# Kernel optimization log

Hardware: AMD Instinct MI355X
Metric: run time of the kernel (lower is better)

The kernel has to match this reference:

```python
import jax, jax.numpy as jnp
import numpy as np

N, M, E, C_IN, C_OUT = 100000, 20000, 1600000, 128, 128


def _safe_inv(d):
    # 1/d with 0 where d==0 (matches PyG D[D==inf]=0), grad-safe
    safe = jnp.where(d > 0, d, 1.0)
    return jnp.where(d > 0, 1.0 / safe, 0.0)


def _hconv(x, node_idx, edge_idx, hw, W, b):
    # PyG HypergraphConv, use_attention=False, heads=1:
    # X' = D^{-1} H B^{-1} H^T (X Theta) + bias, D uses hyperedge_weight
    xt = x @ W  # [N, C_OUT]
    D = jax.ops.segment_sum(hw[edge_idx], node_idx, num_segments=N)
    Dinv = _safe_inv(D)  # [N]
    Bc = jax.ops.segment_sum(jnp.ones((E,), dtype=x.dtype), edge_idx, num_segments=M)
    Binv = _safe_inv(Bc)  # [M]
    # node -> hyperedge (message weighted by B^{-1} of target edge)
    e = jax.ops.segment_sum(Binv[edge_idx][:, None] * xt[node_idx], edge_idx, num_segments=M)
    # hyperedge -> node (message weighted by D^{-1} of target node)
    out = jax.ops.segment_sum(Dinv[node_idx][:, None] * e[edge_idx], node_idx, num_segments=N)
    return out + b


def setup_inputs() -> dict:
    key = jax.random.key(0)
    ks = jax.random.split(key, 12)
    x = jax.random.normal(ks[0], (N, C_IN), dtype=jnp.float32)
    node_idx = jax.random.randint(ks[1], (E,), 0, N, dtype=jnp.int32)
    edge_idx = jax.random.randint(ks[2], (E,), 0, M, dtype=jnp.int32)
    hyperedge_index = jnp.stack([node_idx, edge_idx])
    hyperedge_weight = jax.random.uniform(ks[3], (M,), dtype=jnp.float32) + 0.5
    hyperedge_attr = jax.random.normal(ks[4], (M, C_IN), dtype=jnp.float32)
    batch = jnp.zeros((N,), dtype=jnp.int32)
    s1 = 1.0 / np.sqrt(C_IN)
    s2 = 1.0 / np.sqrt(C_OUT)
    W1 = jax.random.uniform(ks[5], (C_IN, C_OUT), minval=-s1, maxval=s1, dtype=jnp.float32)
    W2 = jax.random.uniform(ks[6], (C_OUT, C_OUT), minval=-s2, maxval=s2, dtype=jnp.float32)
    W3 = jax.random.uniform(ks[7], (C_OUT, C_OUT), minval=-s2, maxval=s2, dtype=jnp.float32)
    b1 = jax.random.uniform(ks[8], (C_OUT,), minval=-s1, maxval=s1, dtype=jnp.float32)
    b2 = jax.random.uniform(ks[9], (C_OUT,), minval=-s2, maxval=s2, dtype=jnp.float32)
    b3 = jax.random.uniform(ks[10], (C_OUT,), minval=-s2, maxval=s2, dtype=jnp.float32)
    return {"x": x, "hyperedge_index": hyperedge_index, "hyperedge_weight": hyperedge_weight,
            "hyperedge_attr": hyperedge_attr, "batch": batch,
            "W1": W1, "b1": b1, "W2": W2, "b2": b2, "W3": W3, "b3": b3}


def reference(x, hyperedge_index, hyperedge_weight, hyperedge_attr, batch,
              W1, b1, W2, b2, W3, b3):
    node_idx = hyperedge_index[0]
    edge_idx = hyperedge_index[1]
    # dropout is identity in eval mode; hyperedge_attr/batch unused (no attention)
    h = jax.nn.relu(_hconv(x, node_idx, edge_idx, hyperedge_weight, W1, b1))
    h = jax.nn.relu(_hconv(h, node_idx, edge_idx, hyperedge_weight, W2, b2))
    h = jax.nn.relu(_hconv(h, node_idx, edge_idx, hyperedge_weight, W3, b3))
    return h
```

## Files before the change

kernel.cpp:

```cpp
#include <hip/hip_runtime.h>
#include <hip/hip_fp16.h>

#define NN 100000
#define MM 20000
#define EE 1600000

#define NBLK_E 256
#define CHUNK_E (EE / NBLK_E)
#define NBLK_N 128
#define CHUNK_N (EE / NBLK_N)
#define NRANGE2 50000

#define SCAN_BLOCK 256
#define SCAN_ITEMS 8
#define SCAN_TILE (SCAN_BLOCK * SCAN_ITEMS)
#define NB_E ((MM + SCAN_TILE - 1) / SCAN_TILE)
#define NB_N ((NN + SCAN_TILE - 1) / SCAN_TILE)
#define NB_TOT (NB_E + NB_N)

static inline size_t align256(size_t x) { return (x + 255) & ~(size_t)255; }

struct alignas(8) half4 { __half2 lo, hi; };

__device__ __forceinline__ float4 h4_to_f4(half4 v) {
  float2 a = __half22float2(v.lo);
  float2 b = __half22float2(v.hi);
  return make_float4(a.x, a.y, b.x, b.y);
}
__device__ __forceinline__ half4 f4_to_h4(float4 v) {
  half4 r;
  r.lo = __float22half2_rn(make_float2(v.x, v.y));
  r.hi = __float22half2_rn(make_float2(v.z, v.w));
  return r;
}

__global__ __launch_bounds__(256) void cvt_f2h_kernel(
    const float* __restrict__ in, __half* __restrict__ out, int n4) {
  int i = blockIdx.x * 256 + threadIdx.x;
  int stride = gridDim.x * 256;
  for (; i < n4; i += stride) {
    float4 v = ((const float4*)in)[i];
    ((half4*)out)[i] = f4_to_h4(v);
  }
}

__global__ __launch_bounds__(256) void ehist_kernel(
    const int* __restrict__ edge_idx,
    unsigned short* __restrict__ bcnt_e, unsigned short* __restrict__ lrank_e) {
  extern __shared__ int hist[];
  int b = blockIdx.x;
  for (int k = threadIdx.x; k < MM; k += 256) hist[k] = 0;
  __syncthreads();
  int lo = b * CHUNK_E, hi = lo + CHUNK_E;
  for (int i = lo + threadIdx.x; i < hi; i += 256) {
    int e = edge_idx[i];
    int r = atomicAdd(&hist[e], 1);
    lrank_e[i] = (unsigned short)r;
  }
  __syncthreads();
  unsigned short* row = bcnt_e + (size_t)b * MM;
  for (int k = threadIdx.x; k < MM / 2; k += 256) {
    ushort2 w;
    w.x = (unsigned short)hist[2 * k];
    w.y = (unsigned short)hist[2 * k + 1];
    ((ushort2*)row)[k] = w;
  }
}

__global__ __launch_bounds__(256) void nhist_kernel(
    const int* __restrict__ node_idx,
    unsigned short* __restrict__ bcnt_n, unsigned short* __restrict__ lrank_n) {
  extern __shared__ unsigned int histp[];
  int b = blockIdx.x;
  int lo = b * CHUNK_N, hi = lo + CHUNK_N;
  unsigned short* row = bcnt_n + (size_t)b * NN;
  for (int p = 0; p < 2; ++p) {
    int base = p * NRANGE2;
    for (int k = threadIdx.x; k < NRANGE2 / 2; k += 256) histp[k] = 0;
    __syncthreads();
    for (int i = lo + threadIdx.x; i < hi; i += 256) {
      int n = node_idx[i] - base;
      if ((unsigned)n < (unsigned)NRANGE2) {
        unsigned add = (n & 1) ? 0x10000u : 1u;
        unsigned old = atomicAdd(&histp[n >> 1], add);
        lrank_n[i] = (unsigned short)((old >> ((n & 1) * 16)) & 0xFFFFu);
      }
    }
    __syncthreads();
    for (int k = threadIdx.x; k < NRANGE2 / 2; k += 256) {
      unsigned w = histp[k];
      ushort2 o;
      o.x = (unsigned short)(w & 0xFFFFu);
      o.y = (unsigned short)(w >> 16);
      ((ushort2*)(row + base))[k] = o;
    }
    __syncthreads();
  }
}

__global__ __launch_bounds__(256) void colscan_kernel(
    unsigned short* __restrict__ bcnt_e, unsigned short* __restrict__ bcnt_n,
    int* __restrict__ ecnt, int* __restrict__ ncnt) {
  int i = blockIdx.x * 256 + threadIdx.x;
  if (i < MM) {
    int run = 0;
#pragma unroll 8
    for (int b = 0; b < NBLK_E; ++b) {
      size_t idx = (size_t)b * MM + i;
      int v = bcnt_e[idx];
      bcnt_e[idx] = (unsigned short)run;
      run += v;
    }
    ecnt[i] = run;
  } else if (i < MM + NN) {
    int n = i - MM;
    int run = 0;
#pragma unroll 8
    for (int b = 0; b < NBLK_N; ++b) {
      size_t idx = (size_t)b * NN + n;
      int v = bcnt_n[idx];
      bcnt_n[idx] = (unsigned short)run;
      run += v;
    }
    ncnt[n] = run;
  }
}

__global__ __launch_bounds__(SCAN_BLOCK) void scan_partial_kernel(
    const int* __restrict__ ecnt, const int* __restrict__ ncnt,
    int* __restrict__ eptr, int* __restrict__ nptr, int* __restrict__ bsum) {
  __shared__ int lds[SCAN_BLOCK];
  int b = blockIdx.x;
  const int* cnt; int* ptr; int len; int lb;
  if (b < NB_E) { cnt = ecnt; ptr = eptr; len = MM; lb = b; }
  else          { cnt = ncnt; ptr = nptr; len = NN; lb = b - NB_E; }
  int t = threadIdx.x;
  int lo = lb * SCAN_TILE + t * SCAN_ITEMS;
  int v[SCAN_ITEMS];
  int s = 0;
#pragma unroll
  for (int j = 0; j < SCAN_ITEMS; ++j) {
    int idx = lo + j;
    v[j] = (idx < len) ? cnt[idx] : 0;
    s += v[j];
  }
  lds[t] = s;
  __syncthreads();
  for (int d = 1; d < SCAN_BLOCK; d <<= 1) {
    int o = (t >= d) ? lds[t - d] : 0;
    __syncthreads();
    lds[t] += o;
    __syncthreads();
  }
  int run = lds[t] - s;
#pragma unroll
  for (int j = 0; j < SCAN_ITEMS; ++j) {
    int idx = lo + j;
    if (idx < len) ptr[idx] = run;
    run += v[j];
  }
  if (t == SCAN_BLOCK - 1) bsum[b] = lds[t];
}

__global__ void scan_bsum_kernel(int* __restrict__ bsum) {
  int t = threadIdx.x;
  if (t == 0) {
    int run = 0;
    for (int i = 0; i < NB_E; ++i) { int c = bsum[i]; bsum[i] = run; run += c; }
  } else if (t == 1) {
    int run = 0;
    for (int i = NB_E; i < NB_TOT; ++i) { int c = bsum[i]; bsum[i] = run; run += c; }
  }
}

__global__ __launch_bounds__(SCAN_BLOCK) void scan_fixup_kernel(
    int* __restrict__ eptr, int* __restrict__ nptr,
    const int* __restrict__ ecnt, const int* __restrict__ bsum,
    float* __restrict__ Binv) {
  int b = blockIdx.x;
  int* ptr; int len; int lb; bool isE;
  if (b < NB_E) { ptr = eptr; len = MM; lb = b; isE = true; }
  else          { ptr = nptr; len = NN; lb = b - NB_E; isE = false; }
  int boff = bsum[b];
  int t = threadIdx.x;
  int lo = lb * SCAN_TILE + t * SCAN_ITEMS;
#pragma unroll
  for (int j = 0; j < SCAN_ITEMS; ++j) {
    int idx = lo + j;
    if (idx < len) {
      ptr[idx] += boff;
      if (isE) {
        int c = ecnt[idx];
        Binv[idx] = (c > 0) ? 1.0f / (float)c : 0.0f;
      }
    }
  }
  if (b == 0 && t == 0) { eptr[MM] = EE; nptr[NN] = EE; }
}

__global__ __launch_bounds__(256) void fill2_kernel(
    const int* __restrict__ node_idx, const int* __restrict__ edge_idx,
    const int* __restrict__ eptr, const int* __restrict__ nptr,
    const unsigned short* __restrict__ bcnt_e,
    const unsigned short* __restrict__ bcnt_n,
    const unsigned short* __restrict__ lrank_e,
    const unsigned short* __restrict__ lrank_n,
    int* __restrict__ edge_nodes, int* __restrict__ node_edges) {
  int i = blockIdx.x * 256 + threadIdx.x;
  if (i >= EE) return;
  int e = edge_idx[i];
  int n = node_idx[i];
  int be = i / CHUNK_E;
  int bn = i / CHUNK_N;
  int slotE = eptr[e] + (int)bcnt_e[(size_t)be * MM + e] + (int)lrank_e[i];
  edge_nodes[slotE] = n;
  int slotN = nptr[n] + (int)bcnt_n[(size_t)bn * NN + n] + (int)lrank_n[i];
  node_edges[slotN] = e;
}

__global__ __launch_bounds__(256) void dinv_csr_kernel(
    const int* __restrict__ nptr, const int* __restrict__ node_edges,
    const float* __restrict__ hw, float* __restrict__ Dinv) {
  int n = blockIdx.x * 256 + threadIdx.x;
  if (n >= NN) return;
  int lo = nptr[n], hi = nptr[n + 1];
  float d = 0.0f;
  for (int j = lo; j < hi; ++j) d += hw[node_edges[j]];
  Dinv[n] = (d > 0.0f) ? 1.0f / d : 0.0f;
}

__device__ __forceinline__ void fma4(float4& acc, float s, const float4& m) {
  acc.x += s * m.x;
  acc.y += s * m.y;
  acc.z += s * m.z;
  acc.w += s * m.w;
}

__global__ __launch_bounds__(256) void gemm128_kernel(
    const __half* __restrict__ X, const float* __restrict__ W,
    __half* __restrict__ Y, int nrows) {
  __shared__ float Wl[128 * 128];
  float4* Wl4 = (float4*)Wl;
  const float4* W4 = (const float4*)W;
  for (int i = threadIdx.x; i < 128 * 32; i += 256) Wl4[i] = W4[i];
  __syncthreads();

  int tc = threadIdx.x & 15;
  int tr = threadIdx.x >> 4;
  int base = blockIdx.x * 64;
  int r[4];
  bool v[4];
#pragma unroll
  for (int j = 0; j < 4; ++j) {
    int rr = base + tr + j * 16;
    v[j] = rr < nrows;
    r[j] = v[j] ? rr : 0;
  }
  float4 acc[4][2];
#pragma unroll
  for (int j = 0; j < 4; ++j) {
    acc[j][0] = make_float4(0.f, 0.f, 0.f, 0.f);
    acc[j][1] = make_float4(0.f, 0.f, 0.f, 0.f);
  }
#pragma unroll 4
  for (int k4 = 0; k4 < 32; ++k4) {
    float4 xv[4];
#pragma unroll
    for (int j = 0; j < 4; ++j)
      xv[j] = h4_to_f4(((const half4*)X)[(size_t)r[j] * 32 + k4]);
#pragma unroll
    for (int kk = 0; kk < 4; ++kk) {
      float4 wva = Wl4[(k4 * 4 + kk) * 32 + tc];
      float4 wvb = Wl4[(k4 * 4 + kk) * 32 + 16 + tc];
#pragma unroll
      for (int j = 0; j < 4; ++j) {
        float xk = ((const float*)&xv[j])[kk];
        fma4(acc[j][0], xk, wva);
        fma4(acc[j][1], xk, wvb);
      }
    }
  }
#pragma unroll
  for (int j = 0; j < 4; ++j) {
    if (v[j]) {
      ((half4*)Y)[(size_t)r[j] * 32 + tc] = f4_to_h4(acc[j][0]);
      ((half4*)Y)[(size_t)r[j] * 32 + 16 + tc] = f4_to_h4(acc[j][1]);
    }
  }
}

__global__ __launch_bounds__(256) void edge_agg_kernel(
    const __half* __restrict__ hin, const int* __restrict__ eptr,
    const int* __restrict__ edge_nodes, const float* __restrict__ Binv,
    __half* __restrict__ eout) {
  int half_id = threadIdx.x >> 5;
  int lane = threadIdx.x & 31;
  int m = blockIdx.x * 8 + half_id;
  if (m >= MM) return;
  int lo = eptr[m], hi = eptr[m + 1];
  const half4* h4p = (const half4*)hin;
  float4 acc = make_float4(0.f, 0.f, 0.f, 0.f);
  int j = lo;
  for (; j + 8 <= hi; j += 8) {
    int idx[8];
#pragma unroll
    for (int u = 0; u < 8; ++u) idx[u] = edge_nodes[j + u];
    float4 s[8];
#pragma unroll
    for (int u = 0; u < 8; ++u) s[u] = h4_to_f4(h4p[(size_t)idx[u] * 32 + lane]);
    acc.x += ((s[0].x + s[1].x) + (s[2].x + s[3].x)) + ((s[4].x + s[5].x) + (s[6].x + s[7].x));
    acc.y += ((s[0].y + s[1].y) + (s[2].y + s[3].y)) + ((s[4].y + s[5].y) + (s[6].y + s[7].y));
    acc.z += ((s[0].z + s[1].z) + (s[2].z + s[3].z)) + ((s[4].z + s[5].z) + (s[6].z + s[7].z));
    acc.w += ((s[0].w + s[1].w) + (s[2].w + s[3].w)) + ((s[4].w + s[5].w) + (s[6].w + s[7].w));
  }
  for (; j < hi; ++j) {
    int n = edge_nodes[j];
    float4 a = h4_to_f4(h4p[(size_t)n * 32 + lane]);
    acc.x += a.x; acc.y += a.y; acc.z += a.z; acc.w += a.w;
  }
  float bi = Binv[m];
  acc.x *= bi; acc.y *= bi; acc.z *= bi; acc.w *= bi;
  ((half4*)eout)[(size_t)m * 32 + lane] = f4_to_h4(acc);
}

__device__ __forceinline__ void strow_q(float* Y, size_t row, int q, float4 v) {
  ((float4*)Y)[row * 32 + q] = v;
}
__device__ __forceinline__ void strow_q(__half* Y, size_t row, int q, float4 v) {
  ((half4*)Y)[row * 32 + q] = f4_to_h4(v);
}

template <typename TOUT>
__global__ __launch_bounds__(256) void node_agg_half_kernel(
    const __half* __restrict__ ein, const int* __restrict__ nptr,
    const int* __restrict__ node_edges, const float* __restrict__ Dinv,
    const float* __restrict__ bias, TOUT* __restrict__ out, int c4) {
  int g = threadIdx.x >> 4;
  int gl = threadIdx.x & 15;
  int n = blockIdx.x * 16 + g;
  int q = c4 + gl;
  int lo = nptr[n], hi = nptr[n + 1];
  const half4* e4 = (const half4*)ein;
  float4 acc = make_float4(0.f, 0.f, 0.f, 0.f);
  int j = lo;
  for (; j + 4 <= hi; j += 4) {
    int m0 = node_edges[j + 0];
    int m1 = node_edges[j + 1];
    int m2 = node_edges[j + 2];
    int m3 = node_edges[j + 3];
    float4 a = h4_to_f4(e4[(size_t)m0 * 32 + q]);
    float4 b = h4_to_f4(e4[(size_t)m1 * 32 + q]);
    float4 c = h4_to_f4(e4[(size_t)m2 * 32 + q]);
    float4 d = h4_to_f4(e4[(size_t)m3 * 32 + q]);
    acc.x += (a.x + b.x) + (c.x + d.x);
    acc.y += (a.y + b.y) + (c.y + d.y);
    acc.z += (a.z + b.z) + (c.z + d.z);
    acc.w += (a.w + b.w) + (c.w + d.w);
  }
  for (; j < hi; ++j) {
    int m = node_edges[j];
    float4 a = h4_to_f4(e4[(size_t)m * 32 + q]);
    acc.x += a.x; acc.y += a.y; acc.z += a.z; acc.w += a.w;
  }
  float di = Dinv[n];
  float4 bb = ((const float4*)bias)[q];
  float4 rv;
  rv.x = fmaxf(di * acc.x + bb.x, 0.f);
  rv.y = fmaxf(di * acc.y + bb.y, 0.f);
  rv.z = fmaxf(di * acc.z + bb.z, 0.f);
  rv.w = fmaxf(di * acc.w + bb.w, 0.f);
  strow_q(out, (size_t)n, q, rv);
}

extern "C" void kernel_launch(void* const* d_in, const int* in_sizes, int n_in,
                              void* d_out, int out_size, void* d_ws, size_t ws_size,
                              hipStream_t stream) {
  const float* x = (const float*)d_in[0];
  const int* hidx = (const int*)d_in[1];
  const int* node_idx = hidx;
  const int* edge_idx = hidx + EE;
  const float* hw = (const float*)d_in[2];
  const float* W1 = (const float*)d_in[5];
  const float* b1 = (const float*)d_in[6];
  const float* W2 = (const float*)d_in[7];
  const float* b2 = (const float*)d_in[8];
  const float* W3 = (const float*)d_in[9];
  const float* b3 = (const float*)d_in[10];
  float* out = (float*)d_out;

  char* ws = (char*)d_ws;
  size_t off = 0;
  auto alloc = [&](size_t bytes) -> char* {
    char* p = ws + off;
    off = align256(off + bytes);
    return p;
  };
  __half* xh   = (__half*)alloc(sizeof(__half) * (size_t)NN * 128);
  __half* h    = (__half*)alloc(sizeof(__half) * (size_t)NN * 128);
  __half* eraw = (__half*)alloc(sizeof(__half) * (size_t)MM * 128);
  __half* et   = (__half*)alloc(sizeof(__half) * (size_t)MM * 128);
  unsigned short* bcnt_e = (unsigned short*)alloc(sizeof(short) * (size_t)NBLK_E * MM);
  unsigned short* bcnt_n = (unsigned short*)alloc(sizeof(short) * (size_t)NBLK_N * NN);
  unsigned short* lrank_e = (unsigned short*)alloc(sizeof(short) * (size_t)EE);
  unsigned short* lrank_n = (unsigned short*)alloc(sizeof(short) * (size_t)EE);
  int*   ecnt  = (int*)alloc(sizeof(int) * MM);
  int*   ncnt  = (int*)alloc(sizeof(int) * NN);
  int*   eptr  = (int*)alloc(sizeof(int) * (MM + 1));
  int*   nptr  = (int*)alloc(sizeof(int) * (NN + 1));
  int*   bsum  = (int*)alloc(sizeof(int) * NB_TOT);
  float* Binv  = (float*)alloc(sizeof(float) * MM);
  float* Dinv  = (float*)alloc(sizeof(float) * NN);
  int* edge_nodes = (int*)alloc(sizeof(int) * (size_t)EE);
  int* node_edges = (int*)alloc(sizeof(int) * (size_t)EE);
  (void)ws_size; (void)in_sizes; (void)n_in; (void)out_size;

  ehist_kernel<<<NBLK_E, 256, MM * sizeof(int), stream>>>(edge_idx, bcnt_e, lrank_e);
  nhist_kernel<<<NBLK_N, 256, (NRANGE2 / 2) * sizeof(int), stream>>>(node_idx, bcnt_n, lrank_n);
  colscan_kernel<<<(MM + NN + 255) / 256, 256, 0, stream>>>(bcnt_e, bcnt_n, ecnt, ncnt);
  scan_partial_kernel<<<NB_TOT, SCAN_BLOCK, 0, stream>>>(ecnt, ncnt, eptr, nptr, bsum);
  scan_bsum_kernel<<<1, 64, 0, stream>>>(bsum);
  scan_fixup_kernel<<<NB_TOT, SCAN_BLOCK, 0, stream>>>(eptr, nptr, ecnt, bsum, Binv);
  fill2_kernel<<<(EE + 255) / 256, 256, 0, stream>>>(node_idx, edge_idx, eptr, nptr,
                                                     bcnt_e, bcnt_n, lrank_e, lrank_n,
                                                     edge_nodes, node_edges);
  dinv_csr_kernel<<<(NN + 255) / 256, 256, 0, stream>>>(nptr, node_edges, hw, Dinv);
  cvt_f2h_kernel<<<1024, 256, 0, stream>>>(x, xh, NN * 32);

  const int gemmE_grid = (MM + 63) / 64;
  const int eagg_grid = MM / 8;
  const int nagg_grid = NN / 16;

  edge_agg_kernel<<<eagg_grid, 256, 0, stream>>>(xh, eptr, edge_nodes, Binv, eraw);
  gemm128_kernel<<<gemmE_grid, 256, 0, stream>>>(eraw, W1, et, MM);
  node_agg_half_kernel<__half><<<nagg_grid, 256, 0, stream>>>(et, nptr, node_edges, Dinv, b1, h, 0);
  node_agg_half_kernel<__half><<<nagg_grid, 256, 0, stream>>>(et, nptr, node_edges, Dinv, b1, h, 16);
  edge_agg_kernel<<<eagg_grid, 256, 0, stream>>>(h, eptr, edge_nodes, Binv, eraw);
  gemm128_kernel<<<gemmE_grid, 256, 0, stream>>>(eraw, W2, et, MM);
  node_agg_half_kernel<__half><<<nagg_grid, 256, 0, stream>>>(et, nptr, node_edges, Dinv, b2, xh, 0);
  node_agg_half_kernel<__half><<<nagg_grid, 256, 0, stream>>>(et, nptr, node_edges, Dinv, b2, xh, 16);
  edge_agg_kernel<<<eagg_grid, 256, 0, stream>>>(xh, eptr, edge_nodes, Binv, eraw);
  gemm128_kernel<<<gemmE_grid, 256, 0, stream>>>(eraw, W3, et, MM);
  node_agg_half_kernel<float><<<nagg_grid, 256, 0, stream>>>(et, nptr, node_edges, Dinv, b3, out, 0);
  node_agg_half_kernel<float><<<nagg_grid, 256, 0, stream>>>(et, nptr, node_edges, Dinv, b3, out, 16);
}
```

Measured before the change: 600.3 us.

## Store node features in channel-panel layout for cache-local edge aggregation

Node feature tensors are now stored as 8 channel panels of 16 halfs each, panel-major across all nodes. The edge aggregation kernel launches one grid slice per panel, so each pass gathers from a 3.2MB panel that can stay in cache. Each gather is a 32-byte slice, and 8 edges are processed in parallel per 32-lane group with a shuffle reduction at the end. The cost is 8x more launched blocks and re-reading the CSR indices once per panel, plus shorter memory transactions per gather.

```diff
diff --git a/kernel.cpp b/kernel.cpp
--- a/kernel.cpp
+++ b/kernel.cpp
@@ -4,6 +4,10 @@
 #define NN 100000
 #define MM 20000
 #define EE 1600000
+
+#define NPANEL 8
+#define EPB 8
+#define PASS_BLOCKS (MM / EPB)
 
 #define NBLK_E 256
 #define CHUNK_E (EE / NBLK_E)
@@ -34,13 +38,21 @@
   return r;
 }
 
-__global__ __launch_bounds__(256) void cvt_f2h_kernel(
-    const float* __restrict__ in, __half* __restrict__ out, int n4) {
+__device__ __forceinline__ void st_node(__half* Y, size_t n, int q, float4 v) {
+  ((half4*)Y)[(((size_t)(q >> 2)) * NN + n) * 4 + (q & 3)] = f4_to_h4(v);
+}
+__device__ __forceinline__ void st_node(float* Y, size_t n, int q, float4 v) {
+  ((float4*)Y)[n * 32 + q] = v;
+}
+
+__global__ __launch_bounds__(256) void cvt_f2h_panel_kernel(
+    const float* __restrict__ in, __half* __restrict__ out) {
   int i = blockIdx.x * 256 + threadIdx.x;
   int stride = gridDim.x * 256;
-  for (; i < n4; i += stride) {
+  for (; i < NN * 32; i += stride) {
+    int n = i >> 5, q = i & 31;
     float4 v = ((const float4*)in)[i];
-    ((half4*)out)[i] = f4_to_h4(v);
+    st_node(out, (size_t)n, q, v);
   }
 }
 
@@ -289,45 +301,36 @@
   }
 }
 
-__global__ __launch_bounds__(256) void edge_agg_kernel(
-    const __half* __restrict__ hin, const int* __restrict__ eptr,
-    const int* __restrict__ edge_nodes, const float* __restrict__ Binv,
-    __half* __restrict__ eout) {
+__global__ __launch_bounds__(256) void edge_agg_panel_kernel(
+    const __half* __restrict__ hp,
+    const int* __restrict__ eptr, const int* __restrict__ edge_nodes,
+    const float* __restrict__ Binv, __half* __restrict__ eout) {
+  int p = blockIdx.x / PASS_BLOCKS;
+  int eb = blockIdx.x % PASS_BLOCKS;
   int half_id = threadIdx.x >> 5;
-  int lane = threadIdx.x & 31;
-  int m = blockIdx.x * 8 + half_id;
-  if (m >= MM) return;
+  int l = threadIdx.x & 31;
+  int m = eb * EPB + half_id;
   int lo = eptr[m], hi = eptr[m + 1];
-  const half4* h4p = (const half4*)hin;
+  int piece = l & 3;
+  const half4* base = (const half4*)hp + (size_t)p * NN * 4;
   float4 acc = make_float4(0.f, 0.f, 0.f, 0.f);
-  int j = lo;
-  for (; j + 8 <= hi; j += 8) {
-    int idx[8];
-#pragma unroll
-    for (int u = 0; u < 8; ++u) idx[u] = edge_nodes[j + u];
-    float4 s[8];
-#pragma unroll
-    for (int u = 0; u < 8; ++u) s[u] = h4_to_f4(h4p[(size_t)idx[u] * 32 + lane]);
-    acc.x += ((s[0].x + s[1].x) + (s[2].x + s[3].x)) + ((s[4].x + s[5].x) + (s[6].x + s[7].x));
-    acc.y += ((s[0].y + s[1].y) + (s[2].y + s[3].y)) + ((s[4].y + s[5].y) + (s[6].y + s[7].y));
-    acc.z += ((s[0].z + s[1].z) + (s[2].z + s[3].z)) + ((s[4].z + s[5].z) + (s[6].z + s[7].z));
-    acc.w += ((s[0].w + s[1].w) + (s[2].w + s[3].w)) + ((s[4].w + s[5].w) + (s[6].w + s[7].w));
-  }
-  for (; j < hi; ++j) {
+  for (int j = lo + (l >> 2); j < hi; j += 8) {
     int n = edge_nodes[j];
-    float4 a = h4_to_f4(h4p[(size_t)n * 32 + lane]);
+    float4 a = h4_to_f4(base[(size_t)n * 4 + piece]);
     acc.x += a.x; acc.y += a.y; acc.z += a.z; acc.w += a.w;
   }
-  float bi = Binv[m];
-  acc.x *= bi; acc.y *= bi; acc.z *= bi; acc.w *= bi;
-  ((half4*)eout)[(size_t)m * 32 + lane] = f4_to_h4(acc);
-}
-
-__device__ __forceinline__ void strow_q(float* Y, size_t row, int q, float4 v) {
-  ((float4*)Y)[row * 32 + q] = v;
-}
-__device__ __forceinline__ void strow_q(__half* Y, size_t row, int q, float4 v) {
-  ((half4*)Y)[row * 32 + q] = f4_to_h4(v);
+#pragma unroll
+  for (int mask = 4; mask <= 16; mask <<= 1) {
+    acc.x += __shfl_xor(acc.x, mask, 64);
+    acc.y += __shfl_xor(acc.y, mask, 64);
+    acc.z += __shfl_xor(acc.z, mask, 64);
+    acc.w += __shfl_xor(acc.w, mask, 64);
+  }
+  if ((l >> 2) == 0) {
+    float bi = Binv[m];
+    acc.x *= bi; acc.y *= bi; acc.z *= bi; acc.w *= bi;
+    ((half4*)eout)[(size_t)m * 32 + p * 4 + piece] = f4_to_h4(acc);
+  }
 }
 
 template <typename TOUT>
@@ -369,7 +372,7 @@
   rv.y = fmaxf(di * acc.y + bb.y, 0.f);
   rv.z = fmaxf(di * acc.z + bb.z, 0.f);
   rv.w = fmaxf(di * acc.w + bb.w, 0.f);
-  strow_q(out, (size_t)n, q, rv);
+  st_node(out, (size_t)n, q, rv);
 }
 
 extern "C" void kernel_launch(void* const* d_in, const int* in_sizes, int n_in,
@@ -424,21 +427,21 @@
                                                      bcnt_e, bcnt_n, lrank_e, lrank_n,
                                                      edge_nodes, node_edges);
   dinv_csr_kernel<<<(NN + 255) / 256, 256, 0, stream>>>(nptr, node_edges, hw, Dinv);
-  cvt_f2h_kernel<<<1024, 256, 0, stream>>>(x, xh, NN * 32);
+  cvt_f2h_panel_kernel<<<1024, 256, 0, stream>>>(x, xh);
 
   const int gemmE_grid = (MM + 63) / 64;
-  const int eagg_grid = MM / 8;
+  const int eagg_grid = NPANEL * PASS_BLOCKS;
   const int nagg_grid = NN / 16;
 
-  edge_agg_kernel<<<eagg_grid, 256, 0, stream>>>(xh, eptr, edge_nodes, Binv, eraw);
+  edge_agg_panel_kernel<<<eagg_grid, 256, 0, stream>>>(xh, eptr, edge_nodes, Binv, eraw);
   gemm128_kernel<<<gemmE_grid, 256, 0, stream>>>(eraw, W1, et, MM);
   node_agg_half_kernel<__half><<<nagg_grid, 256, 0, stream>>>(et, nptr, node_edges, Dinv, b1, h, 0);
   node_agg_half_kernel<__half><<<nagg_grid, 256, 0, stream>>>(et, nptr, node_edges, Dinv, b1, h, 16);
-  edge_agg_kernel<<<eagg_grid, 256, 0, stream>>>(h, eptr, edge_nodes, Binv, eraw);
+  edge_agg_panel_kernel<<<eagg_grid, 256, 0, stream>>>(h, eptr, edge_nodes, Binv, eraw);
   gemm128_kernel<<<gemmE_grid, 256, 0, stream>>>(eraw, W2, et, MM);
   node_agg_half_kernel<__half><<<nagg_grid, 256, 0, stream>>>(et, nptr, node_edges, Dinv, b2, xh, 0);
   node_agg_half_kernel<__half><<<nagg_grid, 256, 0, stream>>>(et, nptr, node_edges, Dinv, b2, xh, 16);
-  edge_agg_kernel<<<eagg_grid, 256, 0, stream>>>(xh, eptr, edge_nodes, Binv, eraw);
+  edge_agg_panel_kernel<<<eagg_grid, 256, 0, stream>>>(xh, eptr, edge_nodes, Binv, eraw);
   gemm128_kernel<<<gemmE_grid, 256, 0, stream>>>(eraw, W3, et, MM);
   node_agg_half_kernel<float><<<nagg_grid, 256, 0, stream>>>(et, nptr, node_edges, Dinv, b3, out, 0);
   node_agg_half_kernel<float><<<nagg_grid, 256, 0, stream>>>(et, nptr, node_edges, Dinv, b3, out, 16);
```

After: 727.2 us. +21.1%, slower.

## Split CSR fill into per-chunk LDS-staged kernels and merge node-agg halves

Applied to the files above, without the earlier changes.

The combined fill kernel is split into separate edge and node fill kernels. Each block handles one histogram chunk and stages its per-block count row in shared memory, replacing scattered global reads of bcnt. The node fill loads its row in two 50000-entry slices to fit LDS, so the chunk's indices are scanned twice. Separately, the two channel-half node aggregation launches per layer become a single launch with twice the grid, which removes launch overhead but changes the order in which blocks reuse cached edge rows.

```diff
diff --git a/kernel.cpp b/kernel.cpp
--- a/kernel.cpp
+++ b/kernel.cpp
@@ -10,6 +10,7 @@
 #define NBLK_N 128
 #define CHUNK_N (EE / NBLK_N)
 #define NRANGE2 50000
+#define NRANGE_F 50000
 
 #define SCAN_BLOCK 256
 #define SCAN_ITEMS 8
@@ -198,24 +199,50 @@
   if (b == 0 && t == 0) { eptr[MM] = EE; nptr[NN] = EE; }
 }
 
-__global__ __launch_bounds__(256) void fill2_kernel(
+__global__ __launch_bounds__(256) void fill_edge_kernel(
     const int* __restrict__ node_idx, const int* __restrict__ edge_idx,
-    const int* __restrict__ eptr, const int* __restrict__ nptr,
+    const int* __restrict__ eptr,
     const unsigned short* __restrict__ bcnt_e,
+    const unsigned short* __restrict__ lrank_e,
+    int* __restrict__ edge_nodes) {
+  __shared__ unsigned short rowb[MM];
+  int b = blockIdx.x;
+  const unsigned short* src = bcnt_e + (size_t)b * MM;
+  for (int k = threadIdx.x; k < MM / 2; k += 256)
+    ((ushort2*)rowb)[k] = ((const ushort2*)src)[k];
+  __syncthreads();
+  int lo = b * CHUNK_E, hi = lo + CHUNK_E;
+  for (int i = lo + threadIdx.x; i < hi; i += 256) {
+    int e = edge_idx[i];
+    int slot = eptr[e] + (int)rowb[e] + (int)lrank_e[i];
+    edge_nodes[slot] = node_idx[i];
+  }
+}
+
+__global__ __launch_bounds__(256) void fill_node_kernel(
+    const int* __restrict__ node_idx, const int* __restrict__ edge_idx,
+    const int* __restrict__ nptr,
     const unsigned short* __restrict__ bcnt_n,
-    const unsigned short* __restrict__ lrank_e,
     const unsigned short* __restrict__ lrank_n,
-    int* __restrict__ edge_nodes, int* __restrict__ node_edges) {
-  int i = blockIdx.x * 256 + threadIdx.x;
-  if (i >= EE) return;
-  int e = edge_idx[i];
-  int n = node_idx[i];
-  int be = i / CHUNK_E;
-  int bn = i / CHUNK_N;
-  int slotE = eptr[e] + (int)bcnt_e[(size_t)be * MM + e] + (int)lrank_e[i];
-  edge_nodes[slotE] = n;
-  int slotN = nptr[n] + (int)bcnt_n[(size_t)bn * NN + n] + (int)lrank_n[i];
-  node_edges[slotN] = e;
+    int* __restrict__ node_edges) {
+  extern __shared__ unsigned short rowslice[];
+  int b = blockIdx.x;
+  int lo = b * CHUNK_N, hi = lo + CHUNK_N;
+  const unsigned short* row = bcnt_n + (size_t)b * NN;
+  for (int p = 0; p < 2; ++p) {
+    int base = p * NRANGE_F;
+    for (int k = threadIdx.x; k < NRANGE_F / 2; k += 256)
+      ((ushort2*)rowslice)[k] = ((const ushort2*)(row + base))[k];
+    __syncthreads();
+    for (int i = lo + threadIdx.x; i < hi; i += 256) {
+      int n = node_idx[i] - base;
+      if ((unsigned)n < (unsigned)NRANGE_F) {
+        int slot = nptr[n + base] + (int)rowslice[n] + (int)lrank_n[i];
+        node_edges[slot] = edge_idx[i];
+      }
+    }
+    __syncthreads();
+  }
 }
 
 __global__ __launch_bounds__(256) void dinv_csr_kernel(
@@ -334,10 +361,13 @@
 __global__ __launch_bounds__(256) void node_agg_half_kernel(
     const __half* __restrict__ ein, const int* __restrict__ nptr,
     const int* __restrict__ node_edges, const float* __restrict__ Dinv,
-    const float* __restrict__ bias, TOUT* __restrict__ out, int c4) {
+    const float* __restrict__ bias, TOUT* __restrict__ out) {
+  int nb = NN / 16;
+  int c4 = (blockIdx.x >= nb) ? 16 : 0;
+  int eb = (blockIdx.x >= nb) ? blockIdx.x - nb : blockIdx.x;
   int g = threadIdx.x >> 4;
   int gl = threadIdx.x & 15;
-  int n = blockIdx.x * 16 + g;
+  int n = eb * 16 + g;
   int q = c4 + gl;
   int lo = nptr[n], hi = nptr[n + 1];
   const half4* e4 = (const half4*)ein;
@@ -420,26 +450,24 @@
   scan_partial_kernel<<<NB_TOT, SCAN_BLOCK, 0, stream>>>(ecnt, ncnt, eptr, nptr, bsum);
   scan_bsum_kernel<<<1, 64, 0, stream>>>(bsum);
   scan_fixup_kernel<<<NB_TOT, SCAN_BLOCK, 0, stream>>>(eptr, nptr, ecnt, bsum, Binv);
-  fill2_kernel<<<(EE + 255) / 256, 256, 0, stream>>>(node_idx, edge_idx, eptr, nptr,
-                                                     bcnt_e, bcnt_n, lrank_e, lrank_n,
-                                                     edge_nodes, node_edges);
+  fill_edge_kernel<<<NBLK_E, 256, 0, stream>>>(node_idx, edge_idx, eptr,
+                                               bcnt_e, lrank_e, edge_nodes);
+  fill_node_kernel<<<NBLK_N, 256, NRANGE_F * sizeof(short), stream>>>(
+      node_idx, edge_idx, nptr, bcnt_n, lrank_n, node_edges);
   dinv_csr_kernel<<<(NN + 255) / 256, 256, 0, stream>>>(nptr, node_edges, hw, Dinv);
   cvt_f2h_kernel<<<1024, 256, 0, stream>>>(x, xh, NN * 32);
 
   const int gemmE_grid = (MM + 63) / 64;
   const int eagg_grid = MM / 8;
-  const int nagg_grid = NN / 16;
+  const int nagg_grid = 2 * (NN / 16);
 
   edge_agg_kernel<<<eagg_grid, 256, 0, stream>>>(xh, eptr, edge_nodes, Binv, eraw);
   gemm128_kernel<<<gemmE_grid, 256, 0, stream>>>(eraw, W1, et, MM);
-  node_agg_half_kernel<__half><<<nagg_grid, 256, 0, stream>>>(et, nptr, node_edges, Dinv, b1, h, 0);
-  node_agg_half_kernel<__half><<<nagg_grid, 256, 0, stream>>>(et, nptr, node_edges, Dinv, b1, h, 16);
+  node_agg_half_kernel<__half><<<nagg_grid, 256, 0, stream>>>(et, nptr, node_edges, Dinv, b1, h);
   edge_agg_kernel<<<eagg_grid, 256, 0, stream>>>(h, eptr, edge_nodes, Binv, eraw);
   gemm128_kernel<<<gemmE_grid, 256, 0, stream>>>(eraw, W2, et, MM);
-  node_agg_half_kernel<__half><<<nagg_grid, 256, 0, stream>>>(et, nptr, node_edges, Dinv, b2, xh, 0);
-  node_agg_half_kernel<__half><<<nagg_grid, 256, 0, stream>>>(et, nptr, node_edges, Dinv, b2, xh, 16);
+  node_agg_half_kernel<__half><<<nagg_grid, 256, 0, stream>>>(et, nptr, node_edges, Dinv, b2, xh);
   edge_agg_kernel<<<eagg_grid, 256, 0, stream>>>(xh, eptr, edge_nodes, Binv, eraw);
   gemm128_kernel<<<gemmE_grid, 256, 0, stream>>>(eraw, W3, et, MM);
-  node_agg_half_kernel<float><<<nagg_grid, 256, 0, stream>>>(et, nptr, node_edges, Dinv, b3, out, 0);
-  node_agg_half_kernel<float><<<nagg_grid, 256, 0, stream>>>(et, nptr, node_edges, Dinv, b3, out, 16);
-}
+  node_agg_half_kernel<float><<<nagg_grid, 256, 0, stream>>>(et, nptr, node_edges, Dinv, b3, out);
+}
```

Result: no change. 610.0 us (+1.6%).
